# Kernel tuning notes

Hardware: AMD Instinct MI355X
Metric: run time of the kernel (lower is better)

Reference implementation:

```python
import jax, jax.numpy as jnp
import numpy as np

N, E, D_IN, D_H, D_OUT, L = 100000, 1000000, 128, 64, 40, 7
MSG_EPS = 1e-7   # GENConv message epsilon
BN_EPS = 1e-5    # torch BatchNorm1d eps
T = 1.0          # softmax temperature (learn_t=False)


def _segment_softmax(logits, seg, n):
    # numerically stable softmax over edges grouped by destination node
    m = jax.ops.segment_max(logits, seg, num_segments=n)
    e = jnp.exp(logits - m[seg])
    s = jax.ops.segment_sum(e, seg, num_segments=n)
    return e / (s[seg] + 1e-16)


def _gen_conv(h, src, dst, W, b):
    # GENConv, aggr='softmax_sg', mlp_layers=1, msg_norm=False
    msg = jax.nn.relu(h[src]) + MSG_EPS                 # [E, D_H]
    w = jax.lax.stop_gradient(_segment_softmax(msg * T, dst, N))
    agg = jax.ops.segment_sum(w * msg, dst, num_segments=N)  # [N, D_H]
    return (h + agg) @ W + b


def _batch_norm(h, gamma, beta):
    mu = jnp.mean(h, axis=0)
    var = jnp.mean(jnp.square(h - mu), axis=0)  # biased var (training mode)
    return gamma * (h - mu) * jax.lax.rsqrt(var + BN_EPS) + beta


def setup_inputs() -> dict:
    key = jax.random.key(0)
    ks = jax.random.split(key, 6)
    x = jax.random.normal(ks[0], (N, D_IN), dtype=jnp.float32)
    edge_index = jax.random.randint(ks[1], (2, E), 0, N, dtype=jnp.int64)
    W_enc = jax.random.normal(ks[2], (D_IN, D_H), dtype=jnp.float32) / np.float32(np.sqrt(D_IN))
    b_enc = jnp.zeros((D_H,), jnp.float32)
    Wg = jax.random.normal(ks[3], (L, D_H, D_H), dtype=jnp.float32) / np.float32(np.sqrt(D_H))
    bg = jnp.zeros((L, D_H), jnp.float32)
    gamma = jnp.ones((L, D_H), jnp.float32)
    beta = jnp.zeros((L, D_H), jnp.float32)
    W_pred = jax.random.normal(ks[4], (D_H, D_OUT), dtype=jnp.float32) / np.float32(np.sqrt(D_H))
    b_pred = jnp.zeros((D_OUT,), jnp.float32)
    return {"x": x, "edge_index": edge_index, "W_enc": W_enc, "b_enc": b_enc,
            "Wg": Wg, "bg": bg, "gamma": gamma, "beta": beta,
            "W_pred": W_pred, "b_pred": b_pred}


def reference(x, edge_index, W_enc, b_enc, Wg, bg, gamma, beta, W_pred, b_pred):
    src, dst = edge_index[0], edge_index[1]
    h = x @ W_enc + b_enc                               # node encoder
    h = _gen_conv(h, src, dst, Wg[0], bg[0])            # first conv (res+)
    for layer in range(1, L):                            # BN->ReLU->Conv->Res
        h2 = jax.nn.relu(_batch_norm(h, gamma[layer - 1], beta[layer - 1]))
        h = _gen_conv(h2, src, dst, Wg[layer], bg[layer]) + h
    h = jax.nn.relu(_batch_norm(h, gamma[L - 1], beta[L - 1]))
    logits = h @ W_pred + b_pred
    return jax.nn.log_softmax(logits, axis=-1)
```

## Files before the change

### kernel.cpp

```cpp
#include <hip/hip_runtime.h>
#include <math.h>

#define NN 100000
#define NE 1000000
#define DH 64
#define DIN 128
#define DOUT 40
#define NL 7
#define SCAN_B 1024
#define NBLK ((NN + SCAN_B - 1) / SCAN_B)
#define NGRP (NN / 16)
#define LBLK ((NGRP + 3) / 4)
#define COLB_CAP (NE + 8 * NN + 64)
#define QS 16.0f
#define IQS 0.0625f

typedef _Float16 v8h __attribute__((ext_vector_type(8)));
typedef float v4f __attribute__((ext_vector_type(4)));

__global__ __launch_bounds__(256) void k_count(const int* __restrict__ dst,
                                               int* __restrict__ cnt,
                                               int* __restrict__ pi) {
  int i = blockIdx.x * 256 + threadIdx.x;
  if (i < NE) pi[i] = atomicAdd(&cnt[dst[i]], 1);
}

__global__ __launch_bounds__(SCAN_B) void k_scan1(const int* __restrict__ cnt,
                                                  int* __restrict__ rp8,
                                                  int* __restrict__ bsum) {
  __shared__ int buf[SCAN_B];
  int i = blockIdx.x * SCAN_B + threadIdx.x;
  int v = (i < NN) ? ((cnt[i] + 7) & ~7) : 0;
  buf[threadIdx.x] = v;
  __syncthreads();
  for (int off = 1; off < SCAN_B; off <<= 1) {
    int t = (threadIdx.x >= off) ? buf[threadIdx.x - off] : 0;
    __syncthreads();
    buf[threadIdx.x] += t;
    __syncthreads();
  }
  if (i < NN) rp8[i] = buf[threadIdx.x] - v;
  if (threadIdx.x == SCAN_B - 1) bsum[blockIdx.x] = buf[SCAN_B - 1];
}

__global__ __launch_bounds__(128) void k_scan2(int* __restrict__ bsum) {
  __shared__ int buf[128];
  int v = (threadIdx.x < NBLK) ? bsum[threadIdx.x] : 0;
  buf[threadIdx.x] = v;
  __syncthreads();
  for (int off = 1; off < 128; off <<= 1) {
    int t = (threadIdx.x >= off) ? buf[threadIdx.x - off] : 0;
    __syncthreads();
    buf[threadIdx.x] += t;
    __syncthreads();
  }
  if (threadIdx.x < NBLK) bsum[threadIdx.x] = buf[threadIdx.x] - v;
}

__global__ __launch_bounds__(SCAN_B) void k_scan3(int* __restrict__ rp8,
                                                  const int* __restrict__ bsum) {
  int i = blockIdx.x * SCAN_B + threadIdx.x;
  if (i < NN) rp8[i] += bsum[blockIdx.x];
}

__global__ __launch_bounds__(256) void k_place(const int* __restrict__ src,
                                               const int* __restrict__ dst,
                                               const int* __restrict__ rp8,
                                               const int* __restrict__ pi,
                                               int* __restrict__ colb) {
  int i = blockIdx.x * 256 + threadIdx.x;
  if (i < NE)
    colb[rp8[dst[i]] + pi[i]] = src[i] * DH + DH;
}

__global__ __launch_bounds__(256) void k_enc_mfma(const float* __restrict__ x,
                                                  const float* __restrict__ W,
                                                  const float* __restrict__ b,
                                                  float* __restrict__ h) {
  __shared__ _Float16 Atile[4][2048];
  const int tid = threadIdx.x;
  const int w = tid >> 6, lane = tid & 63;
  const int gid = blockIdx.x * 4 + w;
  if (gid >= NGRP) return;
  const int row = lane & 15, hi = lane >> 4;

  v8h bf[4][4];
#pragma unroll
  for (int kt = 0; kt < 4; ++kt)
#pragma unroll
    for (int ct = 0; ct < 4; ++ct)
#pragma unroll
      for (int j = 0; j < 8; ++j)
        bf[kt][ct][j] = (_Float16)W[(kt * 32 + hi * 8 + j) * DH + ct * 16 + row];

  const int base = gid * 16;
  _Float16* At = &Atile[w][0];
#pragma unroll 4
  for (int i = 0; i < 16; ++i) {
    float v0 = x[(size_t)(base + i) * DIN + lane];
    float v1 = x[(size_t)(base + i) * DIN + 64 + lane];
    int swi = (i & 7) << 4;
    At[(i * 256 + ((lane * 2) ^ swi)) >> 1] = (_Float16)v0;
    At[(i * 256 + 128 + ((lane * 2) ^ swi)) >> 1] = (_Float16)v1;
  }
  const int sw = (row & 7) << 4;
  v8h a[4];
#pragma unroll
  for (int kt = 0; kt < 4; ++kt) {
    int off = (kt & 1) * 64 + hi * 16;
    a[kt] = *(const v8h*)&At[(row * 256 + (kt >> 1) * 128 + (off ^ sw)) >> 1];
  }
  v4f c0 = {0, 0, 0, 0}, c1 = {0, 0, 0, 0}, c2 = {0, 0, 0, 0}, c3 = {0, 0, 0, 0};
#pragma unroll
  for (int kt = 0; kt < 4; ++kt) {
    c0 = __builtin_amdgcn_mfma_f32_16x16x32_f16(a[kt], bf[kt][0], c0, 0, 0, 0);
    c1 = __builtin_amdgcn_mfma_f32_16x16x32_f16(a[kt], bf[kt][1], c1, 0, 0, 0);
    c2 = __builtin_amdgcn_mfma_f32_16x16x32_f16(a[kt], bf[kt][2], c2, 0, 0, 0);
    c3 = __builtin_amdgcn_mfma_f32_16x16x32_f16(a[kt], bf[kt][3], c3, 0, 0, 0);
  }
  float b0 = b[row], b1 = b[16 + row], b2 = b[32 + row], b3 = b[48 + row];
#pragma unroll
  for (int reg = 0; reg < 4; ++reg) {
    size_t o = (size_t)(base + hi * 4 + reg) * DH;
    h[o + row] = c0[reg] + b0;
    h[o + 16 + row] = c1[reg] + b1;
    h[o + 32 + row] = c2[reg] + b2;
    h[o + 48 + row] = c3[reg] + b3;
  }
}

__global__ __launch_bounds__(256) void k_msg(const float* __restrict__ h,
                                             const float* __restrict__ stats_in,
                                             const float* __restrict__ gamma,
                                             const float* __restrict__ beta,
                                             unsigned char* __restrict__ msg) {
  int lane = threadIdx.x & 63;
  float scale = 1.f, shift = 0.f;
  if (stats_in) {
    float mu = stats_in[lane] * (1.0f / NN);
    float var = stats_in[64 + lane] * (1.0f / NN) - mu * mu;
    scale = gamma[lane] * rsqrtf(var + 1e-5f);
    shift = beta[lane] - mu * scale;
  }
  int wid = (blockIdx.x * blockDim.x + threadIdx.x) >> 6;
  int nw = (gridDim.x * blockDim.x) >> 6;
  for (int n = wid; n < NN; n += nw) {
    float r = h[n * DH + lane];
    float v = fmaxf(fmaf(r, scale, shift), 0.f) + 1e-7f;
    msg[DH + n * DH + lane] = (unsigned char)fminf(v * QS + 0.5f, 255.f);
  }
}

__global__ __launch_bounds__(256) void k_layer2(
    const float* __restrict__ h_pre, const unsigned char* __restrict__ msg,
    const int* __restrict__ rp8, const int* __restrict__ cnt,
    const int* __restrict__ colb, const float* __restrict__ stats_in,
    const float* __restrict__ gamma, const float* __restrict__ beta,
    const float* __restrict__ W, const float* __restrict__ b, int add_res,
    float* __restrict__ hout, float* __restrict__ partial) {
  __shared__ _Float16 At[1024];
  __shared__ float Rw[16 * 68];
  const int tid = threadIdx.x;
  const int w = tid >> 6, lane = tid & 63;
  const int row = lane & 15, hi = lane >> 4;
  const int base = blockIdx.x * 16;

  float scale = 1.f, shift = 0.f;
  if (stats_in) {
    float mu = stats_in[lane] * (1.0f / NN);
    float var = stats_in[64 + lane] * (1.0f / NN) - mu * mu;
    scale = gamma[lane] * rsqrtf(var + 1e-5f);
    shift = beta[lane] - mu * scale;
  }
  v8h bf0, bf1;
#pragma unroll
  for (int j = 0; j < 8; ++j) {
    bf0[j] = (_Float16)W[(hi * 8 + j) * DH + w * 16 + row];
    bf1[j] = (_Float16)W[(32 + hi * 8 + j) * DH + w * 16 + row];
  }
  float rawv[4];
#pragma unroll
  for (int k = 0; k < 4; ++k)
    rawv[k] = h_pre[(size_t)(base + w * 4 + k) * DH + lane];

  const unsigned char* mb = msg + lane;
#pragma unroll
  for (int k = 0; k < 4; ++k) {
    int n = base + w * 4 + k;
    int beg = __builtin_amdgcn_readfirstlane(rp8[n]);
    int deg = __builtin_amdgcn_readfirstlane(cnt[n]);
    int pdeg = (deg + 7) & ~7;
    float s = 0.f, t = 0.f;
    for (int j = 0; j < pdeg; j += 8) {
      int cc[8];
#pragma unroll
      for (int q = 0; q < 8; ++q) cc[q] = colb[beg + j + q];
      float vv[8];
#pragma unroll
      for (int q = 0; q < 8; ++q) vv[q] = (float)mb[cc[q]] * IQS;
#pragma unroll
      for (int q = 0; q < 8; ++q) {
        float e = __expf(vv[q]);
        s += e;
        t = fmaf(e, vv[q], t);
      }
    }
    s -= (float)(pdeg - deg);
    float aggv = t / (s + 1e-16f);
    float v = stats_in ? fmaxf(fmaf(rawv[k], scale, shift), 0.f) : rawv[k];
    v += aggv;
    int i = w * 4 + k;
    At[(i * 128 + ((lane * 2) ^ ((i & 7) << 4))) >> 1] = (_Float16)v;
    Rw[i * 68 + lane] = rawv[k];
  }
  __syncthreads();

  const int sw = (row & 7) << 4;
  v8h a0 = *(const v8h*)&At[((row * 128) + ((hi * 16) ^ sw)) >> 1];
  v8h a1 = *(const v8h*)&At[((row * 128) + ((64 + hi * 16) ^ sw)) >> 1];
  v4f c = {0, 0, 0, 0};
  c = __builtin_amdgcn_mfma_f32_16x16x32_f16(a0, bf0, c, 0, 0, 0);
  c = __builtin_amdgcn_mfma_f32_16x16x32_f16(a1, bf1, c, 0, 0, 0);

  float bb = b[w * 16 + row];
  float ss = 0.f, qq = 0.f;
#pragma unroll
  for (int reg = 0; reg < 4; ++reg) {
    size_t o = (size_t)(base + hi * 4 + reg) * DH + w * 16 + row;
    float av = c[reg] + bb;
    if (add_res) av += Rw[(hi * 4 + reg) * 68 + w * 16 + row];
    hout[o] = av;
    ss += av;
    qq = fmaf(av, av, qq);
  }
  ss += __shfl_xor(ss, 16, 64); qq += __shfl_xor(qq, 16, 64);
  ss += __shfl_xor(ss, 32, 64); qq += __shfl_xor(qq, 32, 64);
  if (hi == 0) {
    partial[(size_t)blockIdx.x * 128 + w * 16 + row] = ss;
    partial[(size_t)blockIdx.x * 128 + 64 + w * 16 + row] = qq;
  }
}

__global__ __launch_bounds__(256) void k_red(const float* __restrict__ partial,
                                             float* __restrict__ stats) {
  const int f = blockIdx.x;
  float acc = 0.f;
  for (int i = threadIdx.x; i < NGRP; i += 256)
    acc += partial[(size_t)i * 128 + f];
  __shared__ float buf[256];
  buf[threadIdx.x] = acc;
  __syncthreads();
  for (int off = 128; off >= 1; off >>= 1) {
    if (threadIdx.x < off) buf[threadIdx.x] += buf[threadIdx.x + off];
    __syncthreads();
  }
  if (threadIdx.x == 0) stats[f] = buf[0];
}

__global__ __launch_bounds__(256) void k_pred_mfma(
    const float* __restrict__ h_pre, const float* __restrict__ stats_in,
    const float* __restrict__ gamma, const float* __restrict__ beta,
    const float* __restrict__ Wp, const float* __restrict__ bp,
    float* __restrict__ out) {
  __shared__ _Float16 Atile[4][1024];
  const int tid = threadIdx.x;
  const int w = tid >> 6, lane = tid & 63;
  const int gid = blockIdx.x * 4 + w;
  if (gid >= NGRP) return;
  const int row = lane & 15, hi = lane >> 4;

  float mu = stats_in[lane] * (1.0f / NN);
  float var = stats_in[64 + lane] * (1.0f / NN) - mu * mu;
  float scale = gamma[lane] * rsqrtf(var + 1e-5f);
  float shift = beta[lane] - mu * scale;

  v8h bf[2][3];
#pragma unroll
  for (int kt = 0; kt < 2; ++kt)
#pragma unroll
    for (int ct = 0; ct < 3; ++ct) {
      int n = ct * 16 + row;
#pragma unroll
      for (int j = 0; j < 8; ++j)
        bf[kt][ct][j] =
            (n < DOUT) ? (_Float16)Wp[(kt * 32 + hi * 8 + j) * DOUT + n]
                       : (_Float16)0.f;
    }

  const int base = gid * 16;
  const float* hl = h_pre + lane;
  _Float16* At = &Atile[w][0];
#pragma unroll 4
  for (int i = 0; i < 16; ++i) {
    float raw = hl[(size_t)(base + i) * DH];
    float v = fmaxf(fmaf(raw, scale, shift), 0.f);
    At[(i * 128 + ((lane * 2) ^ ((i & 7) << 4))) >> 1] = (_Float16)v;
  }
  const int sw = (row & 7) << 4;
  v8h a0 = *(const v8h*)&At[((row * 128) + ((hi * 16) ^ sw)) >> 1];
  v8h a1 = *(const v8h*)&At[((row * 128) + ((64 + hi * 16) ^ sw)) >> 1];
  v4f c0 = {0, 0, 0, 0}, c1 = {0, 0, 0, 0}, c2 = {0, 0, 0, 0};
  c0 = __builtin_amdgcn_mfma_f32_16x16x32_f16(a0, bf[0][0], c0, 0, 0, 0);
  c0 = __builtin_amdgcn_mfma_f32_16x16x32_f16(a1, bf[1][0], c0, 0, 0, 0);
  c1 = __builtin_amdgcn_mfma_f32_16x16x32_f16(a0, bf[0][1], c1, 0, 0, 0);
  c1 = __builtin_amdgcn_mfma_f32_16x16x32_f16(a1, bf[1][1], c1, 0, 0, 0);
  c2 = __builtin_amdgcn_mfma_f32_16x16x32_f16(a0, bf[0][2], c2, 0, 0, 0);
  c2 = __builtin_amdgcn_mfma_f32_16x16x32_f16(a1, bf[1][2], c2, 0, 0, 0);

  float bp0 = bp[row], bp1 = bp[16 + row];
  float bp2 = (32 + row < DOUT) ? bp[32 + row] : 0.f;
  bool v2 = (32 + row) < DOUT;
#pragma unroll
  for (int reg = 0; reg < 4; ++reg) {
    float l0 = c0[reg] + bp0;
    float l1 = c1[reg] + bp1;
    float l2 = v2 ? (c2[reg] + bp2) : -INFINITY;
    float xm = fmaxf(fmaxf(l0, l1), l2);
#pragma unroll
    for (int off = 1; off <= 8; off <<= 1) xm = fmaxf(xm, __shfl_xor(xm, off, 64));
    float e = __expf(l0 - xm) + __expf(l1 - xm) + (v2 ? __expf(l2 - xm) : 0.f);
#pragma unroll
    for (int off = 1; off <= 8; off <<= 1) e += __shfl_xor(e, off, 64);
    float ls = xm + __logf(e);
    size_t o = (size_t)(base + hi * 4 + reg) * DOUT;
    out[o + row] = l0 - ls;
    out[o + 16 + row] = l1 - ls;
    if (v2) out[o + 32 + row] = l2 - ls;
  }
}

extern "C" void kernel_launch(void* const* d_in, const int* in_sizes, int n_in,
                              void* d_out, int out_size, void* d_ws, size_t ws_size,
                              hipStream_t stream) {
  const float* x      = (const float*)d_in[0];
  const int*   ei     = (const int*)d_in[1];
  const float* W_enc  = (const float*)d_in[2];
  const float* b_enc  = (const float*)d_in[3];
  const float* Wg     = (const float*)d_in[4];
  const float* bg     = (const float*)d_in[5];
  const float* gamma  = (const float*)d_in[6];
  const float* beta   = (const float*)d_in[7];
  const float* W_pred = (const float*)d_in[8];
  const float* b_pred = (const float*)d_in[9];
  float* out = (float*)d_out;

  const int* src = ei;
  const int* dst = ei + NE;

  char* p = (char*)d_ws;
  auto alloc = [&](size_t bytes) -> void* {
    void* r = (void*)p;
    p += (bytes + 255) & ~(size_t)255;
    return r;
  };
  float*         hA      = (float*)alloc((size_t)NN * DH * 4);
  float*         hB      = (float*)alloc((size_t)NN * DH * 4);
  unsigned char* msg     = (unsigned char*)alloc((size_t)(NN + 1) * DH);
  int*           rp8     = (int*)alloc((size_t)NN * 4);
  int*           pi      = (int*)alloc((size_t)NE * 4);
  int*           cnt     = (int*)alloc((size_t)NN * 4);
  int*           colb    = (int*)alloc((size_t)COLB_CAP * 4);
  int*           bsum    = (int*)alloc((size_t)NBLK * 4);
  float*         stats   = (float*)alloc((size_t)NL * 128 * 4);
  float*         partial = (float*)alloc((size_t)NGRP * 128 * 4);

  hipMemsetAsync(cnt, 0, (size_t)NN * 4, stream);
  hipMemsetAsync(colb, 0, (size_t)COLB_CAP * 4, stream);
  hipMemsetAsync(msg, 0, DH, stream);

  k_count<<<(NE + 255) / 256, 256, 0, stream>>>(dst, cnt, pi);
  k_scan1<<<NBLK, SCAN_B, 0, stream>>>(cnt, rp8, bsum);
  k_scan2<<<1, 128, 0, stream>>>(bsum);
  k_scan3<<<NBLK, SCAN_B, 0, stream>>>(rp8, bsum);
  k_place<<<(NE + 255) / 256, 256, 0, stream>>>(src, dst, rp8, pi, colb);

  k_enc_mfma<<<LBLK, 256, 0, stream>>>(x, W_enc, b_enc, hA);

  const int MSG_BLOCKS = 1024;

  k_msg<<<MSG_BLOCKS, 256, 0, stream>>>(hA, nullptr, nullptr, nullptr, msg);
  k_layer2<<<NGRP, 256, 0, stream>>>(
      hA, msg, rp8, cnt, colb, nullptr, nullptr, nullptr, Wg, bg, 0, hB, partial);
  k_red<<<128, 256, 0, stream>>>(partial, stats);

  float* h = hB;
  float* hn = hA;
  for (int l = 1; l < NL; ++l) {
    const float* st = stats + (size_t)(l - 1) * 128;
    const float* g  = gamma + (size_t)(l - 1) * DH;
    const float* be = beta + (size_t)(l - 1) * DH;
    k_msg<<<MSG_BLOCKS, 256, 0, stream>>>(h, st, g, be, msg);
    k_layer2<<<NGRP, 256, 0, stream>>>(
        h, msg, rp8, cnt, colb, st, g, be,
        Wg + (size_t)l * DH * DH, bg + (size_t)l * DH, 1,
        hn, partial);
    k_red<<<128, 256, 0, stream>>>(partial, stats + (size_t)l * 128);
    float* tmp = h; h = hn; hn = tmp;
  }

  k_pred_mfma<<<LBLK, 256, 0, stream>>>(
      h, stats + (size_t)(NL - 1) * 128,
      gamma + (size_t)(NL - 1) * DH, beta + (size_t)(NL - 1) * DH,
      W_pred, b_pred, out);
}
```

Measured before the change: 503.1 us.

## Fuse scan passes and edge placement with first message kernel, use exp2

Merges the block-sum scan into the add-offset pass, where each block reduces the preceding block sums itself. Also fuses CSR edge placement with the layer-0 message quantization into one launch, using separate block ranges, which removes two kernel launches. In the aggregation loop, exp(q/16) is replaced with a native exp2 on the raw quantized value with a folded constant, and the 1/16 scale is deferred to a single multiply per node. The cost is slightly different rounding and redundant small reductions in each scan block.

```diff
diff --git a/kernel.cpp b/kernel.cpp
--- a/kernel.cpp
+++ b/kernel.cpp
@@ -14,6 +14,15 @@
 #define COLB_CAP (NE + 8 * NN + 64)
 #define QS 16.0f
 #define IQS 0.0625f
+#define K2F 0.09016844f
+#define PLACE_BLOCKS ((NE + 255) / 256)
+#define MSG0_BLOCKS 1024
+
+#if __has_builtin(__builtin_amdgcn_exp2f)
+#define EXP2(x) __builtin_amdgcn_exp2f(x)
+#else
+#define EXP2(x) exp2f(x)
+#endif
 
 typedef _Float16 v8h __attribute__((ext_vector_type(8)));
 typedef float v4f __attribute__((ext_vector_type(4)));
@@ -43,34 +52,20 @@
   if (threadIdx.x == SCAN_B - 1) bsum[blockIdx.x] = buf[SCAN_B - 1];
 }
 
-__global__ __launch_bounds__(128) void k_scan2(int* __restrict__ bsum) {
-  __shared__ int buf[128];
-  int v = (threadIdx.x < NBLK) ? bsum[threadIdx.x] : 0;
-  buf[threadIdx.x] = v;
-  __syncthreads();
-  for (int off = 1; off < 128; off <<= 1) {
-    int t = (threadIdx.x >= off) ? buf[threadIdx.x - off] : 0;
-    __syncthreads();
-    buf[threadIdx.x] += t;
-    __syncthreads();
-  }
-  if (threadIdx.x < NBLK) bsum[threadIdx.x] = buf[threadIdx.x] - v;
-}
-
 __global__ __launch_bounds__(SCAN_B) void k_scan3(int* __restrict__ rp8,
                                                   const int* __restrict__ bsum) {
-  int i = blockIdx.x * SCAN_B + threadIdx.x;
-  if (i < NN) rp8[i] += bsum[blockIdx.x];
-}
-
-__global__ __launch_bounds__(256) void k_place(const int* __restrict__ src,
-                                               const int* __restrict__ dst,
-                                               const int* __restrict__ rp8,
-                                               const int* __restrict__ pi,
-                                               int* __restrict__ colb) {
-  int i = blockIdx.x * 256 + threadIdx.x;
-  if (i < NE)
-    colb[rp8[dst[i]] + pi[i]] = src[i] * DH + DH;
+  __shared__ int buf[128];
+  int tid = threadIdx.x;
+  if (tid < 128)
+    buf[tid] = (tid < NBLK && tid < (int)blockIdx.x) ? bsum[tid] : 0;
+  __syncthreads();
+  for (int off = 64; off >= 1; off >>= 1) {
+    if (tid < off) buf[tid] += buf[tid + off];
+    __syncthreads();
+  }
+  int b = buf[0];
+  int i = blockIdx.x * SCAN_B + tid;
+  if (i < NN) rp8[i] += b;
 }
 
 __global__ __launch_bounds__(256) void k_enc_mfma(const float* __restrict__ x,
@@ -129,19 +124,36 @@
   }
 }
 
+__global__ __launch_bounds__(256) void k_place_msg0(
+    const int* __restrict__ src, const int* __restrict__ dst,
+    const int* __restrict__ rp8, const int* __restrict__ pi,
+    int* __restrict__ colb, const float* __restrict__ h,
+    unsigned char* __restrict__ msg) {
+  int bid = blockIdx.x;
+  if (bid < PLACE_BLOCKS) {
+    int i = bid * 256 + threadIdx.x;
+    if (i < NE) colb[rp8[dst[i]] + pi[i]] = src[i] * DH + DH;
+  } else {
+    int lane = threadIdx.x & 63;
+    int wid = ((bid - PLACE_BLOCKS) * 256 + threadIdx.x) >> 6;
+    int nw = (MSG0_BLOCKS * 256) >> 6;
+    for (int n = wid; n < NN; n += nw) {
+      float v = fmaxf(h[n * DH + lane], 0.f) + 1e-7f;
+      msg[DH + n * DH + lane] = (unsigned char)fminf(v * QS + 0.5f, 255.f);
+    }
+  }
+}
+
 __global__ __launch_bounds__(256) void k_msg(const float* __restrict__ h,
                                              const float* __restrict__ stats_in,
                                              const float* __restrict__ gamma,
                                              const float* __restrict__ beta,
                                              unsigned char* __restrict__ msg) {
   int lane = threadIdx.x & 63;
-  float scale = 1.f, shift = 0.f;
-  if (stats_in) {
-    float mu = stats_in[lane] * (1.0f / NN);
-    float var = stats_in[64 + lane] * (1.0f / NN) - mu * mu;
-    scale = gamma[lane] * rsqrtf(var + 1e-5f);
-    shift = beta[lane] - mu * scale;
-  }
+  float mu = stats_in[lane] * (1.0f / NN);
+  float var = stats_in[64 + lane] * (1.0f / NN) - mu * mu;
+  float scale = gamma[lane] * rsqrtf(var + 1e-5f);
+  float shift = beta[lane] - mu * scale;
   int wid = (blockIdx.x * blockDim.x + threadIdx.x) >> 6;
   int nw = (gridDim.x * blockDim.x) >> 6;
   for (int n = wid; n < NN; n += nw) {
@@ -195,18 +207,18 @@
       int cc[8];
 #pragma unroll
       for (int q = 0; q < 8; ++q) cc[q] = colb[beg + j + q];
-      float vv[8];
-#pragma unroll
-      for (int q = 0; q < 8; ++q) vv[q] = (float)mb[cc[q]] * IQS;
+      float qf[8];
+#pragma unroll
+      for (int q = 0; q < 8; ++q) qf[q] = (float)mb[cc[q]];
 #pragma unroll
       for (int q = 0; q < 8; ++q) {
-        float e = __expf(vv[q]);
+        float e = EXP2(qf[q] * K2F);
         s += e;
-        t = fmaf(e, vv[q], t);
+        t = fmaf(e, qf[q], t);
       }
     }
     s -= (float)(pdeg - deg);
-    float aggv = t / (s + 1e-16f);
+    float aggv = t * IQS / (s + 1e-16f);
     float v = stats_in ? fmaxf(fmaf(rawv[k], scale, shift), 0.f) : rawv[k];
     v += aggv;
     int i = w * 4 + k;
@@ -370,15 +382,15 @@
 
   k_count<<<(NE + 255) / 256, 256, 0, stream>>>(dst, cnt, pi);
   k_scan1<<<NBLK, SCAN_B, 0, stream>>>(cnt, rp8, bsum);
-  k_scan2<<<1, 128, 0, stream>>>(bsum);
   k_scan3<<<NBLK, SCAN_B, 0, stream>>>(rp8, bsum);
-  k_place<<<(NE + 255) / 256, 256, 0, stream>>>(src, dst, rp8, pi, colb);
 
   k_enc_mfma<<<LBLK, 256, 0, stream>>>(x, W_enc, b_enc, hA);
 
+  k_place_msg0<<<PLACE_BLOCKS + MSG0_BLOCKS, 256, 0, stream>>>(
+      src, dst, rp8, pi, colb, hA, msg);
+
   const int MSG_BLOCKS = 1024;
 
-  k_msg<<<MSG_BLOCKS, 256, 0, stream>>>(hA, nullptr, nullptr, nullptr, msg);
   k_layer2<<<NGRP, 256, 0, stream>>>(
       hA, msg, rp8, cnt, colb, nullptr, nullptr, nullptr, Wg, bg, 0, hB, partial);
   k_red<<<128, 256, 0, stream>>>(partial, stats);
```

Result: no change. 498.6 us (-0.9%).
